# Kernel optimization log

Measured on AMD Instinct MI355X. Metric: run time of the kernel, lower is better.

The kernel has to match this reference:

```python
import jax, jax.numpy as jnp
import numpy as np

ALPHA = 0.1  # LeakyReLU negative slope
F_OUT = 128

def _leaky(x):
    return jnp.where(x >= 0, x, ALPHA * x)

def setup_inputs() -> dict:
    key = jax.random.key(0)
    ks = jax.random.split(key, 12)
    B, N, F_IN = 4, 4096, 128
    q = jax.random.normal(ks[0], (B, N, F_IN), jnp.float32)
    k = jax.random.normal(ks[1], (B, N, F_IN), jnp.float32)
    v = jax.random.normal(ks[2], (B, N, F_IN), jnp.float32)
    adj = jax.random.randint(ks[3], (B, N, N), 0, 2, jnp.int32)
    s = 1.0 / np.sqrt(F_IN)
    Wq_w = jax.random.uniform(ks[4], (F_OUT, F_IN), jnp.float32, -s, s)
    Wq_b = jax.random.uniform(ks[5], (F_OUT,), jnp.float32, -s, s)
    Wk_w = jax.random.uniform(ks[6], (F_OUT, F_IN), jnp.float32, -s, s)
    Wk_b = jax.random.uniform(ks[7], (F_OUT,), jnp.float32, -s, s)
    Wv_w = jax.random.uniform(ks[8], (F_OUT, F_IN), jnp.float32, -s, s)
    Wv_b = jax.random.uniform(ks[9], (F_OUT,), jnp.float32, -s, s)
    # xavier_uniform with gain=1.414 on (2F,1)
    lim = 1.414 * np.sqrt(6.0 / (2 * F_OUT + 1))
    a = jax.random.uniform(ks[10], (2 * F_OUT, 1), jnp.float32, -lim, lim)
    so = 1.0 / np.sqrt(F_OUT)
    Wo_w = jax.random.uniform(ks[11], (F_OUT, F_OUT), jnp.float32, -so, so)
    return {"q": q, "k": k, "v": v, "adj": adj, "Wq_w": Wq_w, "Wq_b": Wq_b,
            "Wk_w": Wk_w, "Wk_b": Wk_b, "Wv_w": Wv_w, "Wv_b": Wv_b,
            "a": a, "Wo_w": Wo_w}

def reference(q, k, v, adj, Wq_w, Wq_b, Wk_w, Wk_b, Wv_w, Wv_b, a, Wo_w):
    qp = q @ Wq_w.T + Wq_b                      # (B,N,F)
    kp = k @ Wk_w.T + Wk_b
    vp = v @ Wv_w.T + Wv_b
    Wh1 = qp @ a[:F_OUT]                        # (B,N,1)
    Wh2 = kp @ a[F_OUT:]                        # (B,N,1)
    e = _leaky(Wh1 + jnp.swapaxes(Wh2, 1, 2))   # (B,N,N)
    e = jnp.where(adj > 0, e, jnp.float32(-1e9))
    att = jax.nn.softmax(e, axis=-1)
    h = jnp.einsum('bnm,bmf->bnf', att, vp)     # (B,N,F)
    return _leaky(h @ Wo_w.T)
```

## Files before the change

kernel.cpp:

```cpp
#include <hip/hip_runtime.h>


constexpr int B = 4, N = 4096, F = 128;
constexpr int BN = B * N;
constexpr int BK = 64;
constexpr int SPLITS = 4;
constexpr int JC = N / SPLITS;
constexpr int NIT = JC / BK;
#define ALPHA 0.1f

using float4v = __attribute__((ext_vector_type(4))) float;
using short8 = __attribute__((ext_vector_type(8))) short;
typedef unsigned long long ull;

__device__ __forceinline__ float leaky(float x) { return x >= 0.f ? x : ALPHA * x; }
__device__ __forceinline__ unsigned short f2bf(float x) {
    unsigned u = __float_as_uint(x);
    u = (u + 0x7FFFu + ((u >> 16) & 1u)) >> 16;
    return (unsigned short)u;
}
__device__ __forceinline__ unsigned pack_bf2(float lo, float hi) {
    unsigned a = __float_as_uint(lo), b2 = __float_as_uint(hi);
    a = a + 0x7FFFu + ((a >> 16) & 1u);
    b2 = b2 + 0x7FFFu + ((b2 >> 16) & 1u);
    return __builtin_amdgcn_perm(b2, a, 0x07060302u);
}

__global__ __launch_bounds__(256) void k_pack(const int* __restrict__ adj,
                                              ull* __restrict__ pack) {
    const long long GROUPS = (long long)B * N * N / 256;
    int t = threadIdx.x;
    int lane = t & 63;
    long long gw = ((long long)blockIdx.x * 256 + t) >> 6;
    long long nw = ((long long)gridDim.x * 256) >> 6;
    for (long long g = gw; g < GROUPS; g += nw) {
        long long base = g * 256;
        ull m0 = __ballot(adj[base + lane] != 0);
        ull m1 = __ballot(adj[base + 64 + lane] != 0);
        ull m2 = __ballot(adj[base + 128 + lane] != 0);
        ull m3 = __ballot(adj[base + 192 + lane] != 0);
        if (lane < 4) {
            ull w = (lane == 0) ? m0 : (lane == 1) ? m1 : (lane == 2) ? m2 : m3;
            pack[g * 4 + lane] = w;
        }
    }
}

__global__ __launch_bounds__(256) void k_ptrans(const ull* __restrict__ pack,
                                                ull* __restrict__ packT) {
    __shared__ ull tile[64][65];
    int t = threadIdx.x;
    int blk = blockIdx.x;
    int b = blk >> 6;
    int i0 = (blk & 63) * 64;
#pragma unroll
    for (int u = 0; u < 16; u++) {
        int unit = u * 256 + t;
        tile[unit >> 6][unit & 63] =
            pack[((size_t)b * N + i0 + (unit >> 6)) * 64 + (unit & 63)];
    }
    __syncthreads();
#pragma unroll
    for (int u = 0; u < 16; u++) {
        int unit = u * 256 + t;
        packT[((size_t)b * 64 + (unit >> 6)) * N + i0 + (unit & 63)] =
            tile[unit & 63][unit >> 6];
    }
}

__global__ void k_prep(const float* __restrict__ Wq_w, const float* __restrict__ Wq_b,
                       const float* __restrict__ Wk_w, const float* __restrict__ Wk_b,
                       const float* __restrict__ a, float* __restrict__ c1,
                       float* __restrict__ c2, float* __restrict__ d12) {
    __shared__ float as[2 * F];
    __shared__ float red[2 * F];
    int t = threadIdx.x;
    as[t] = a[t];
    __syncthreads();
    int f = t & 127;
    const float* W = (t < F) ? Wq_w : Wk_w;
    const float* ao = (t < F) ? as : as + F;
    float s = 0.f;
#pragma unroll 8
    for (int o = 0; o < F; o++) s = fmaf(W[o * F + f], ao[o], s);
    if (t < F) c1[f] = s; else c2[f] = s;
    red[t] = (t < F) ? Wq_b[f] * as[f] : Wk_b[f] * as[F + f];
    __syncthreads();
    for (int st = 64; st > 0; st >>= 1) {
        if (f < st) red[t] += red[t + st];
        __syncthreads();
    }
    if (t == 0) d12[0] = red[0];
    if (t == F) d12[1] = red[F];
}

__global__ void k_wh(const float* __restrict__ q, const float* __restrict__ k,
                     const float* __restrict__ c1, const float* __restrict__ c2,
                     const float* __restrict__ d12,
                     float* __restrict__ Wh1, float* __restrict__ Wh2) {
    __shared__ float c1s[F], c2s[F];
    int t = threadIdx.x;
    if (t < F) c1s[t] = c1[t]; else c2s[t - F] = c2[t - F];
    __syncthreads();
    int row = blockIdx.x * 8 + (t >> 5);
    int lane = t & 31;
    float4 q4 = reinterpret_cast<const float4*>(q)[row * 32 + lane];
    float4 k4 = reinterpret_cast<const float4*>(k)[row * 32 + lane];
    float s1 = q4.x * c1s[lane * 4 + 0] + q4.y * c1s[lane * 4 + 1] +
               q4.z * c1s[lane * 4 + 2] + q4.w * c1s[lane * 4 + 3];
    float s2 = k4.x * c2s[lane * 4 + 0] + k4.y * c2s[lane * 4 + 1] +
               k4.z * c2s[lane * 4 + 2] + k4.w * c2s[lane * 4 + 3];
    for (int m = 16; m > 0; m >>= 1) { s1 += __shfl_xor(s1, m); s2 += __shfl_xor(s2, m); }
    if (lane == 0) { Wh1[row] = s1 + d12[0]; Wh2[row] = s2 + d12[1]; }
}

__global__ void k_max2(const float* __restrict__ Wh2, float* __restrict__ M2) {
    int b = blockIdx.x, t = threadIdx.x;
    float m = -1e30f;
    for (int i = t; i < N; i += 256) m = fmaxf(m, Wh2[b * N + i]);
    __shared__ float red[256];
    red[t] = m;
    __syncthreads();
    for (int s = 128; s > 0; s >>= 1) { if (t < s) red[t] = fmaxf(red[t], red[t + s]); __syncthreads(); }
    if (t == 0) M2[b] = red[0];
}

__global__ void k_tab(const float* __restrict__ Wh1, const float* __restrict__ Wh2,
                      const float* __restrict__ M2,
                      float* __restrict__ P1, float* __restrict__ Q1,
                      float* __restrict__ P2, float* __restrict__ Q2) {
    int i = blockIdx.x * 256 + threadIdx.x;
    int b = i >> 12;
    float w1 = Wh1[i], w2 = Wh2[i];
    float mi = leaky(w1 + M2[b]);
    P1[i] = __expf(w1 - mi);
    Q1[i] = __expf(ALPHA * w1 - mi);
    P2[i] = __expf(w2);
    Q2[i] = __expf(ALPHA * w2);
}

__global__ __launch_bounds__(256) void k_vp(const float* __restrict__ v,
                                            const float* __restrict__ Wv_w,
                                            const float* __restrict__ Wv_b,
                                            unsigned short* __restrict__ vpT) {
    __shared__ float vs[32][F];
    __shared__ float Ws[F][129];
    __shared__ unsigned short ts[F][40];
    int t = threadIdx.x;
    int row0g = blockIdx.x * 32;
    int b = row0g >> 12;
    int row0 = row0g & (N - 1);
    {
        const float4* src = reinterpret_cast<const float4*>(v + row0g * F);
        float4* dst = reinterpret_cast<float4*>(&vs[0][0]);
#pragma unroll
        for (int u = 0; u < 4; u++) dst[u * 256 + t] = src[u * 256 + t];
    }
    {
        const float4* src = reinterpret_cast<const float4*>(Wv_w);
#pragma unroll
        for (int u = 0; u < 16; u++) {
            int unit = u * 256 + t;
            int r = unit >> 5, s = unit & 31;
            float4 val = src[unit];
            Ws[r][s * 4 + 0] = val.x; Ws[r][s * 4 + 1] = val.y;
            Ws[r][s * 4 + 2] = val.z; Ws[r][s * 4 + 3] = val.w;
        }
    }
    int f = t & 127, g = t >> 7;
    float bias = Wv_b[f];
    __syncthreads();
    float acc[16];
#pragma unroll
    for (int r = 0; r < 16; r++) acc[r] = bias;
    for (int kk = 0; kk < F; kk++) {
        float wk = Ws[f][kk];
#pragma unroll
        for (int r = 0; r < 16; r++) acc[r] = fmaf(vs[g * 16 + r][kk], wk, acc[r]);
    }
#pragma unroll
    for (int r = 0; r < 16; r++) ts[f][g * 16 + r] = f2bf(acc[r]);
    __syncthreads();
    int fr = t >> 1, hseg = t & 1;
    uint4 d0 = *reinterpret_cast<uint4*>(&ts[fr][hseg * 16]);
    uint4 d1 = *reinterpret_cast<uint4*>(&ts[fr][hseg * 16 + 8]);
    unsigned short* dst = vpT + ((size_t)(b * F + fr) * N + row0 + hseg * 16);
    *reinterpret_cast<uint4*>(dst) = d0;
    *reinterpret_cast<uint4*>(dst + 8) = d1;
}

__global__ __launch_bounds__(256, 2) void k_attn(
    const unsigned short* __restrict__ vpT, const ull* __restrict__ packT,
    const float* __restrict__ Wh1, const float* __restrict__ P1, const float* __restrict__ Q1,
    const float* __restrict__ P2, const float* __restrict__ Q2, const float* __restrict__ Wh2,
    float* __restrict__ h_part, float* __restrict__ den_part) {
    __shared__ __align__(16) unsigned short bs[2][F][72];
    __shared__ __align__(16) float sP2[JC], sQ2[JC], sW2[JC];
    int t = threadIdx.x;
    int idx = blockIdx.x;
    int split = idx & 3;
    int tile = (idx >> 2) & 31;
    int b = idx >> 7;
    int i0 = tile * 128;
    int jb0 = split * JC;
    int widx = t >> 6, lane = t & 63, m = lane & 15, q = lane >> 4;

    {
        reinterpret_cast<float4*>(sP2)[t] = reinterpret_cast<const float4*>(P2 + b * N + jb0)[t];
        reinterpret_cast<float4*>(sQ2)[t] = reinterpret_cast<const float4*>(Q2 + b * N + jb0)[t];
        reinterpret_cast<float4*>(sW2)[t] = reinterpret_cast<const float4*>(Wh2 + b * N + jb0)[t];
    }

    int gi0 = b * N + i0 + widx * 32 + m;
    int gi1 = gi0 + 16;
    float p1a = P1[gi0], q1a = Q1[gi0], t1a = -Wh1[gi0];
    float p1b = P1[gi1], q1b = Q1[gi1], t1b = -Wh1[gi1];

    const ull* pt = packT + ((size_t)b * 64 + (size_t)split * 16) * N + i0 + widx * 32 + m;
    const unsigned short* vb = vpT + (size_t)b * F * N + jb0;

    uint4 sreg[4];
    auto load_stage = [&](int it) {
#pragma unroll
        for (int u = 0; u < 4; u++) {
            int unit = u * 256 + t;
            int r = unit >> 3, s = unit & 7;
            sreg[u] = *reinterpret_cast<const uint4*>(vb + (size_t)r * N + it * BK + s * 8);
        }
    };
    auto write_stage = [&](int pb) {
#pragma unroll
        for (int u = 0; u < 4; u++) {
            int unit = u * 256 + t;
            int r = unit >> 3, s = unit & 7;
            *reinterpret_cast<uint4*>(&bs[pb][r][s * 8]) = sreg[u];
        }
    };

    float4v acc0[8], acc1[8];
#pragma unroll
    for (int nt = 0; nt < 8; nt++) {
        acc0[nt] = (float4v){0.f, 0.f, 0.f, 0.f};
        acc1[nt] = (float4v){0.f, 0.f, 0.f, 0.f};
    }
    float den0 = 0.f, den1 = 0.f;

    auto gen_af = [&](unsigned bt, const float4& x2a, const float4& x2b,
                      const float4& p2a, const float4& p2b, const float4& q2a,
                      const float4& q2b, float p1, float q1, float t1, float& dn) -> short8 {
        float w0 = (bt & 1u)   ? ((x2a.x >= t1) ? p1 * p2a.x : q1 * q2a.x) : 0.f;
        float w1 = (bt & 2u)   ? ((x2a.y >= t1) ? p1 * p2a.y : q1 * q2a.y) : 0.f;
        float w2 = (bt & 4u)   ? ((x2a.z >= t1) ? p1 * p2a.z : q1 * q2a.z) : 0.f;
        float w3 = (bt & 8u)   ? ((x2a.w >= t1) ? p1 * p2a.w : q1 * q2a.w) : 0.f;
        float w4 = (bt & 16u)  ? ((x2b.x >= t1) ? p1 * p2b.x : q1 * q2b.x) : 0.f;
        float w5 = (bt & 32u)  ? ((x2b.y >= t1) ? p1 * p2b.y : q1 * q2b.y) : 0.f;
        float w6 = (bt & 64u)  ? ((x2b.z >= t1) ? p1 * p2b.z : q1 * q2b.z) : 0.f;
        float w7 = (bt & 128u) ? ((x2b.w >= t1) ? p1 * p2b.w : q1 * q2b.w) : 0.f;
        dn += ((w0 + w1) + (w2 + w3)) + ((w4 + w5) + (w6 + w7));
        union { short8 s; uint4 u; } r;
        r.u.x = pack_bf2(w0, w1); r.u.y = pack_bf2(w2, w3);
        r.u.z = pack_bf2(w4, w5); r.u.w = pack_bf2(w6, w7);
        return r.s;
    };

    auto body = [&](int it, int pb, ull pw0, ull pw1, ull& nx0, ull& nx1) {
        if (it + 1 < NIT) {
            load_stage(it + 1);
            nx0 = pt[(size_t)(it + 1) * N];
            nx1 = pt[(size_t)(it + 1) * N + 16];
        }
#pragma unroll
        for (int kh = 0; kh < 2; kh++) {
            int jl = it * BK + kh * 32 + q * 8;
            float4 x2a = *reinterpret_cast<const float4*>(&sW2[jl]);
            float4 x2b = *reinterpret_cast<const float4*>(&sW2[jl + 4]);
            float4 p2a = *reinterpret_cast<const float4*>(&sP2[jl]);
            float4 p2b = *reinterpret_cast<const float4*>(&sP2[jl + 4]);
            float4 q2a = *reinterpret_cast<const float4*>(&sQ2[jl]);
            float4 q2b = *reinterpret_cast<const float4*>(&sQ2[jl + 4]);
            unsigned bt0 = ((unsigned)(pw0 >> (kh * 32)) >> (q * 8)) & 0xFFu;
            unsigned bt1 = ((unsigned)(pw1 >> (kh * 32)) >> (q * 8)) & 0xFFu;
            short8 af0 = gen_af(bt0, x2a, x2b, p2a, p2b, q2a, q2b, p1a, q1a, t1a, den0);
            short8 af1 = gen_af(bt1, x2a, x2b, p2a, p2b, q2a, q2b, p1b, q1b, t1b, den1);
#pragma unroll
            for (int nt = 0; nt < 8; nt++) {
                short8 bf = *reinterpret_cast<const short8*>(&bs[pb][nt * 16 + m][kh * 32 + q * 8]);
                acc0[nt] = __builtin_amdgcn_mfma_f32_16x16x32_bf16(af0, bf, acc0[nt], 0, 0, 0);
                acc1[nt] = __builtin_amdgcn_mfma_f32_16x16x32_bf16(af1, bf, acc1[nt], 0, 0, 0);
            }
        }
        if (it + 1 < NIT) write_stage(pb ^ 1);
        __syncthreads();
    };

    ull pwA0, pwA1, pwB0, pwB1;
    load_stage(0);
    pwA0 = pt[0];
    pwA1 = pt[16];
    write_stage(0);
    __syncthreads();

#pragma unroll 1
    for (int ith = 0; ith < NIT / 2; ith++) {
        body(ith * 2 + 0, 0, pwA0, pwA1, pwB0, pwB1);
        body(ith * 2 + 1, 1, pwB0, pwB1, pwA0, pwA1);
    }

    den0 += __shfl_xor(den0, 16); den0 += __shfl_xor(den0, 32);
    den1 += __shfl_xor(den1, 16); den1 += __shfl_xor(den1, 32);
    float* dp = den_part + (size_t)split * BN;
    if (q == 0) { dp[gi0] = den0; dp[gi1] = den1; }
    float* hp = h_part + (size_t)split * BN * F;
    int orow = b * N + i0 + widx * 32 + q * 4;
#pragma unroll
    for (int nt = 0; nt < 8; nt++)
#pragma unroll
        for (int r = 0; r < 4; r++) {
            hp[(size_t)(orow + r) * F + nt * 16 + m] = acc0[nt][r];
            hp[(size_t)(orow + 16 + r) * F + nt * 16 + m] = acc1[nt][r];
        }
}

__global__ __launch_bounds__(256) void k_out(const float* __restrict__ h_part,
                                             const float* __restrict__ den_part,
                                             const float* __restrict__ Wo_w,
                                             float* __restrict__ out) {
    __shared__ float hs[32][F];
    __shared__ float Ws[F][129];
    int t = threadIdx.x;
    int row0 = blockIdx.x * 32;
    {
        const float4* src = reinterpret_cast<const float4*>(Wo_w);
#pragma unroll
        for (int u = 0; u < 16; u++) {
            int unit = u * 256 + t;
            int r = unit >> 5, s = unit & 31;
            float4 val = src[unit];
            Ws[r][s * 4 + 0] = val.x; Ws[r][s * 4 + 1] = val.y;
            Ws[r][s * 4 + 2] = val.z; Ws[r][s * 4 + 3] = val.w;
        }
    }
#pragma unroll
    for (int u = 0; u < 4; u++) {
        int unit = u * 256 + t;
        int r = unit >> 5, s = unit & 31;
        size_t off = (size_t)(row0 + r) * F + s * 4;
        float4 h0 = *reinterpret_cast<const float4*>(h_part + off);
        float4 h1 = *reinterpret_cast<const float4*>(h_part + (size_t)BN * F + off);
        float4 h2 = *reinterpret_cast<const float4*>(h_part + (size_t)2 * BN * F + off);
        float4 h3 = *reinterpret_cast<const float4*>(h_part + (size_t)3 * BN * F + off);
        float dsum = den_part[row0 + r] + den_part[BN + row0 + r] +
                     den_part[2 * BN + row0 + r] + den_part[3 * BN + row0 + r];
        float inv = 1.f / dsum;
        hs[r][s * 4 + 0] = (h0.x + h1.x + h2.x + h3.x) * inv;
        hs[r][s * 4 + 1] = (h0.y + h1.y + h2.y + h3.y) * inv;
        hs[r][s * 4 + 2] = (h0.z + h1.z + h2.z + h3.z) * inv;
        hs[r][s * 4 + 3] = (h0.w + h1.w + h2.w + h3.w) * inv;
    }
    __syncthreads();
    int f = t & 127, g = t >> 7;
    float acc[16];
#pragma unroll
    for (int r = 0; r < 16; r++) acc[r] = 0.f;
    for (int kk = 0; kk < F; kk++) {
        float wk = Ws[f][kk];
#pragma unroll
        for (int r = 0; r < 16; r++) acc[r] = fmaf(hs[g * 16 + r][kk], wk, acc[r]);
    }
#pragma unroll
    for (int r = 0; r < 16; r++) out[(size_t)(row0 + g * 16 + r) * F + f] = leaky(acc[r]);
}

extern "C" void kernel_launch(void* const* d_in, const int* in_sizes, int n_in,
                              void* d_out, int out_size, void* d_ws, size_t ws_size,
                              hipStream_t stream) {
    const float* q    = (const float*)d_in[0];
    const float* k    = (const float*)d_in[1];
    const float* v    = (const float*)d_in[2];
    const int*   adj  = (const int*)d_in[3];
    const float* Wq_w = (const float*)d_in[4];
    const float* Wq_b = (const float*)d_in[5];
    const float* Wk_w = (const float*)d_in[6];
    const float* Wk_b = (const float*)d_in[7];
    const float* Wv_w = (const float*)d_in[8];
    const float* Wv_b = (const float*)d_in[9];
    const float* a    = (const float*)d_in[10];
    const float* Wo_w = (const float*)d_in[11];
    float* out = (float*)d_out;
    float* ws = (float*)d_ws;

    unsigned short* vpT = (unsigned short*)ws;
    float* h_part   = ws + BN * F / 2;
    float* den_part = h_part + (size_t)SPLITS * BN * F;
    float* Wh1 = den_part + SPLITS * BN;
    float* Wh2 = Wh1 + BN;
    float* P1  = Wh2 + BN;
    float* Q1  = P1 + BN;
    float* P2  = Q1 + BN;
    float* Q2  = P2 + BN;
    float* c1  = Q2 + BN;
    float* c2  = c1 + F;
    float* d12 = c2 + F;
    float* M2  = d12 + 2;
    size_t off = (size_t)((M2 + B) - ws);
    off = (off + 3) & ~(size_t)3;
    ull* pack  = (ull*)(ws + off);
    ull* packT = pack + (size_t)BN * (N / 64);

    k_pack<<<2048, 256, 0, stream>>>(adj, pack);
    k_ptrans<<<B * 64, 256, 0, stream>>>(pack, packT);
    k_prep<<<1, 256, 0, stream>>>(Wq_w, Wq_b, Wk_w, Wk_b, a, c1, c2, d12);
    k_wh<<<BN / 8, 256, 0, stream>>>(q, k, c1, c2, d12, Wh1, Wh2);
    k_max2<<<B, 256, 0, stream>>>(Wh2, M2);
    k_tab<<<BN / 256, 256, 0, stream>>>(Wh1, Wh2, M2, P1, Q1, P2, Q2);
    k_vp<<<BN / 32, 256, 0, stream>>>(v, Wv_w, Wv_b, vpT);
    k_attn<<<B * 32 * SPLITS, 256, 0, stream>>>(vpT, packT, Wh1, P1, Q1, P2, Q2, Wh2,
                                                h_part, den_part);
    k_out<<<BN / 32, 256, 0, stream>>>(h_part, den_part, Wo_w, out);
}
```

Baseline: 523.0 us.

## Double key splits, single-buffer LDS, and raise attention kernel occupancy

Raises the key-dimension split count from 4 to 8, so twice as many attention blocks run, each over a shorter key range. It drops the double-buffered B tile in LDS for a single buffer with an extra barrier per iteration, and raises the launch-bounds occupancy hint from 2 to 4 blocks per CU. The aim is more parallelism and more resident waves to hide latency. The cost is twice as much partial-sum traffic through h_part, a longer reduction loop in k_out, and less overlap between loads and MFMA from the extra syncs.

```diff
diff --git a/kernel.cpp b/kernel.cpp
--- a/kernel.cpp
+++ b/kernel.cpp
@@ -4,7 +4,7 @@
 constexpr int B = 4, N = 4096, F = 128;
 constexpr int BN = B * N;
 constexpr int BK = 64;
-constexpr int SPLITS = 4;
+constexpr int SPLITS = 8;
 constexpr int JC = N / SPLITS;
 constexpr int NIT = JC / BK;
 #define ALPHA 0.1f
@@ -189,23 +189,23 @@
     *reinterpret_cast<uint4*>(dst + 8) = d1;
 }
 
-__global__ __launch_bounds__(256, 2) void k_attn(
+__global__ __launch_bounds__(256, 4) void k_attn(
     const unsigned short* __restrict__ vpT, const ull* __restrict__ packT,
     const float* __restrict__ Wh1, const float* __restrict__ P1, const float* __restrict__ Q1,
     const float* __restrict__ P2, const float* __restrict__ Q2, const float* __restrict__ Wh2,
     float* __restrict__ h_part, float* __restrict__ den_part) {
-    __shared__ __align__(16) unsigned short bs[2][F][72];
+    __shared__ __align__(16) unsigned short bs[F][72];
     __shared__ __align__(16) float sP2[JC], sQ2[JC], sW2[JC];
     int t = threadIdx.x;
     int idx = blockIdx.x;
-    int split = idx & 3;
-    int tile = (idx >> 2) & 31;
-    int b = idx >> 7;
+    int split = idx & 7;
+    int tile = (idx >> 3) & 31;
+    int b = idx >> 8;
     int i0 = tile * 128;
     int jb0 = split * JC;
     int widx = t >> 6, lane = t & 63, m = lane & 15, q = lane >> 4;
 
-    {
+    if (t < 128) {
         reinterpret_cast<float4*>(sP2)[t] = reinterpret_cast<const float4*>(P2 + b * N + jb0)[t];
         reinterpret_cast<float4*>(sQ2)[t] = reinterpret_cast<const float4*>(Q2 + b * N + jb0)[t];
         reinterpret_cast<float4*>(sW2)[t] = reinterpret_cast<const float4*>(Wh2 + b * N + jb0)[t];
@@ -216,7 +216,7 @@
     float p1a = P1[gi0], q1a = Q1[gi0], t1a = -Wh1[gi0];
     float p1b = P1[gi1], q1b = Q1[gi1], t1b = -Wh1[gi1];
 
-    const ull* pt = packT + ((size_t)b * 64 + (size_t)split * 16) * N + i0 + widx * 32 + m;
+    const ull* pt = packT + ((size_t)b * 64 + (size_t)split * 8) * N + i0 + widx * 32 + m;
     const unsigned short* vb = vpT + (size_t)b * F * N + jb0;
 
     uint4 sreg[4];
@@ -228,12 +228,12 @@
             sreg[u] = *reinterpret_cast<const uint4*>(vb + (size_t)r * N + it * BK + s * 8);
         }
     };
-    auto write_stage = [&](int pb) {
+    auto write_stage = [&]() {
 #pragma unroll
         for (int u = 0; u < 4; u++) {
             int unit = u * 256 + t;
             int r = unit >> 3, s = unit & 7;
-            *reinterpret_cast<uint4*>(&bs[pb][r][s * 8]) = sreg[u];
+            *reinterpret_cast<uint4*>(&bs[r][s * 8]) = sreg[u];
         }
     };
 
@@ -263,7 +263,14 @@
         return r.s;
     };
 
-    auto body = [&](int it, int pb, ull pw0, ull pw1, ull& nx0, ull& nx1) {
+    ull pw0 = pt[0], pw1 = pt[16];
+    ull nx0, nx1;
+    load_stage(0);
+    write_stage();
+    __syncthreads();
+
+#pragma unroll 1
+    for (int it = 0; it < NIT; it++) {
         if (it + 1 < NIT) {
             load_stage(it + 1);
             nx0 = pt[(size_t)(it + 1) * N];
@@ -284,26 +291,17 @@
             short8 af1 = gen_af(bt1, x2a, x2b, p2a, p2b, q2a, q2b, p1b, q1b, t1b, den1);
 #pragma unroll
             for (int nt = 0; nt < 8; nt++) {
-                short8 bf = *reinterpret_cast<const short8*>(&bs[pb][nt * 16 + m][kh * 32 + q * 8]);
+                short8 bf = *reinterpret_cast<const short8*>(&bs[nt * 16 + m][kh * 32 + q * 8]);
                 acc0[nt] = __builtin_amdgcn_mfma_f32_16x16x32_bf16(af0, bf, acc0[nt], 0, 0, 0);
                 acc1[nt] = __builtin_amdgcn_mfma_f32_16x16x32_bf16(af1, bf, acc1[nt], 0, 0, 0);
             }
         }
-        if (it + 1 < NIT) write_stage(pb ^ 1);
-        __syncthreads();
-    };
-
-    ull pwA0, pwA1, pwB0, pwB1;
-    load_stage(0);
-    pwA0 = pt[0];
-    pwA1 = pt[16];
-    write_stage(0);
-    __syncthreads();
-
-#pragma unroll 1
-    for (int ith = 0; ith < NIT / 2; ith++) {
-        body(ith * 2 + 0, 0, pwA0, pwA1, pwB0, pwB1);
-        body(ith * 2 + 1, 1, pwB0, pwB1, pwA0, pwA1);
+        if (it + 1 < NIT) {
+            __syncthreads();
+            write_stage();
+            __syncthreads();
+            pw0 = nx0; pw1 = nx1;
+        }
     }
 
     den0 += __shfl_xor(den0, 16); den0 += __shfl_xor(den0, 32);
@@ -345,17 +343,19 @@
         int unit = u * 256 + t;
         int r = unit >> 5, s = unit & 31;
         size_t off = (size_t)(row0 + r) * F + s * 4;
-        float4 h0 = *reinterpret_cast<const float4*>(h_part + off);
-        float4 h1 = *reinterpret_cast<const float4*>(h_part + (size_t)BN * F + off);
-        float4 h2 = *reinterpret_cast<const float4*>(h_part + (size_t)2 * BN * F + off);
-        float4 h3 = *reinterpret_cast<const float4*>(h_part + (size_t)3 * BN * F + off);
-        float dsum = den_part[row0 + r] + den_part[BN + row0 + r] +
-                     den_part[2 * BN + row0 + r] + den_part[3 * BN + row0 + r];
+        float4 hv = *reinterpret_cast<const float4*>(h_part + off);
+        float dsum = den_part[row0 + r];
+#pragma unroll
+        for (int sp = 1; sp < SPLITS; sp++) {
+            float4 hx = *reinterpret_cast<const float4*>(h_part + (size_t)sp * BN * F + off);
+            hv.x += hx.x; hv.y += hx.y; hv.z += hx.z; hv.w += hx.w;
+            dsum += den_part[sp * BN + row0 + r];
+        }
         float inv = 1.f / dsum;
-        hs[r][s * 4 + 0] = (h0.x + h1.x + h2.x + h3.x) * inv;
-        hs[r][s * 4 + 1] = (h0.y + h1.y + h2.y + h3.y) * inv;
-        hs[r][s * 4 + 2] = (h0.z + h1.z + h2.z + h3.z) * inv;
-        hs[r][s * 4 + 3] = (h0.w + h1.w + h2.w + h3.w) * inv;
+        hs[r][s * 4 + 0] = hv.x * inv;
+        hs[r][s * 4 + 1] = hv.y * inv;
+        hs[r][s * 4 + 2] = hv.z * inv;
+        hs[r][s * 4 + 3] = hv.w * inv;
     }
     __syncthreads();
     int f = t & 127, g = t >> 7;
```

Result: slower. 597.0 us (+14.2%).
